# Kernel tuning notes

Hardware: AMD Instinct MI355X
Metric: run time of the kernel (lower is better)

Reference implementation:

```python
import jax, jax.numpy as jnp
import numpy as np

T, N, E = 3, 100000, 1600000
D_IN, D_H, D_OUT = 64, 64, 1


def _linear_params(key, fan_in, fan_out):
    s = 1.0 / np.sqrt(fan_in)
    k1, k2 = jax.random.split(key)
    W = jax.random.uniform(k1, (fan_in, fan_out), jnp.float32, -s, s)
    b = jax.random.uniform(k2, (fan_out,), jnp.float32, -s, s)
    return W, b


def setup_inputs() -> dict:
    key = jax.random.key(0)
    ks = jax.random.split(key, 9)
    x = jax.random.normal(ks[0], (T, N, D_IN), jnp.float32)
    src = jax.random.randint(ks[1], (T, E), 0, N, jnp.int32)
    dst = jax.random.randint(ks[2], (T, E), 0, N, jnp.int32)
    # xavier-uniform initial GCN weight [D_IN, D_H]
    lim = np.sqrt(6.0 / (D_IN + D_H))
    initial_weight = jax.random.uniform(ks[3], (D_IN, D_H), jnp.float32, -lim, lim)
    Wz, bz = _linear_params(ks[4], D_IN + D_H, D_H)  # update gate
    Wr, br = _linear_params(ks[5], D_IN + D_H, D_H)  # reset gate
    Wh, bh = _linear_params(ks[6], D_IN + D_H, D_H)  # htilda
    Wp, bp = _linear_params(ks[7], D_IN, D_IN)        # pool_proj
    Wo, bo = _linear_params(ks[8], D_H, D_OUT)        # out
    return dict(x=x, src=src, dst=dst, initial_weight=initial_weight,
                Wz=Wz, bz=bz, Wr=Wr, br=br, Wh=Wh, bh=bh,
                Wp=Wp, bp=bp, Wo=Wo, bo=bo)


def reference(x, src, dst, initial_weight, Wz, bz, Wr, br, Wh, bh, Wp, bp, Wo, bo):
    n_nodes = x.shape[1]
    ones_e = jnp.ones((x.shape[2] * 0 + src.shape[1],), jnp.float32)  # [E]

    def step(w, snap):
        xt, st, dt = snap  # [N, D_IN], [E], [E]
        # pooled graph context -> MatGRU weight evolution
        ctx = jnp.mean(xt, axis=0) @ Wp + bp            # [D_IN]
        inp = jnp.broadcast_to(ctx, (D_IN, D_IN))       # inputs.repeat(prev_w.size(0),1)
        xc = jnp.concatenate([inp, w], axis=1)          # [D_IN, D_IN+D_H]
        z = jax.nn.sigmoid(xc @ Wz + bz)
        r = jax.nn.sigmoid(xc @ Wr + br)
        gc = jnp.concatenate([inp, r * w], axis=1)
        h_tilde = jnp.tanh(gc @ Wh + bh)
        w_new = z * w + (1.0 - z) * h_tilde             # [D_IN, D_H]
        # GCN norm: deg = sum of (unit) edge weights per dst, clamp_min 1
        deg = jax.ops.segment_sum(ones_e, dt, num_segments=n_nodes)
        deg = jnp.maximum(deg, 1.0)
        norm = (1.0 / deg)[dt]                          # [E]
        # u_mul_e -> sum aggregation
        agg = jax.ops.segment_sum(xt[st] * norm[:, None], dt, num_segments=n_nodes)
        h = agg @ w_new                                 # [N, D_H]
        out = h @ Wo + bo                               # [N, D_OUT]
        return w_new, out

    w_final, outs = jax.lax.scan(step, initial_weight, (x, src, dst))
    return outs, w_final
```

## Files before the change

### kernel.cpp

```cpp
#include <hip/hip_runtime.h>
#include <math.h>

#define T_STEPS 3
#define N_NODES 100000
#define N_EDGES 1600000
#define N_E4    (N_EDGES / 4)
#define D 64

#define CS_BLOCKS 782

#define BKT_BITS 9
#define BKT_SIZE 512
#define NBKT 196
#define NBKT_PAD 256
#define QSCALE 65536.0f
#define QINV   (1.0f / 65536.0f)

#define SC_EPB 4096
#define SC_I4  1024
#define SC_CHUNKS 391

#define GR_PAD 68

#define PACK_SCALE 1048576.0f
#define PACK_INV   (1.0f / 1048576.0f)


__global__ __launch_bounds__(256) void colsum_part_kernel(const float* __restrict__ x,
                                                          float* __restrict__ colsumP) {
    const int t = blockIdx.y;
    const int tid = threadIdx.x;
    const int q = tid & 15;
    const int g = tid >> 4;
    const float4* xt = (const float4*)(x + (size_t)t * N_NODES * D);
    const int base = blockIdx.x * 128;
    float sx = 0.f, sy = 0.f, sz = 0.f, sw = 0.f;
#pragma unroll
    for (int it = 0; it < 8; ++it) {
        const int r = base + g + 16 * it;
        if (r < N_NODES) {
            const float4 vv = xt[(size_t)r * 16 + q];
            sx += vv.x; sy += vv.y; sz += vv.z; sw += vv.w;
        }
    }
    __shared__ float red[16][64];
    red[g][q * 4 + 0] = sx;
    red[g][q * 4 + 1] = sy;
    red[g][q * 4 + 2] = sz;
    red[g][q * 4 + 3] = sw;
    __syncthreads();
    if (tid < 64) {
        float s = 0.f;
#pragma unroll
        for (int gg = 0; gg < 16; ++gg) s += red[gg][tid];
        colsumP[((size_t)t * CS_BLOCKS + blockIdx.x) * 64 + tid] = s;
    }
}

__global__ __launch_bounds__(256) void hist_chunk_kernel(const int* __restrict__ dst,
                                                         unsigned* __restrict__ histChunk) {
    const int t = blockIdx.y;
    const int c = blockIdx.x;
    const int tid = threadIdx.x;
    __shared__ unsigned h[NBKT_PAD];
    h[tid] = 0;
    __syncthreads();
    const int4* dp = (const int4*)(dst + (size_t)t * N_EDGES);
#pragma unroll
    for (int it = 0; it < 4; ++it) {
        const int i4 = c * SC_I4 + it * 256 + tid;
        if (i4 < N_E4) {
            const int4 d = dp[i4];
            atomicAdd(&h[d.x >> BKT_BITS], 1u);
            atomicAdd(&h[d.y >> BKT_BITS], 1u);
            atomicAdd(&h[d.z >> BKT_BITS], 1u);
            atomicAdd(&h[d.w >> BKT_BITS], 1u);
        }
    }
    __syncthreads();
    histChunk[((size_t)t * SC_CHUNKS + c) * NBKT_PAD + tid] = h[tid];
}

__device__ __forceinline__ float fast_sigmoid(float v) {
    return 1.f / (1.f + __expf(-v));
}
__device__ __forceinline__ float fast_tanh(float v) {
    return 1.f - 2.f / (__expf(2.f * v) + 1.f);
}

__global__ __launch_bounds__(256) void gru_rows_kernel(
    const float* __restrict__ colsumP, const float* __restrict__ iw,
    const float* __restrict__ Wz, const float* __restrict__ bz,
    const float* __restrict__ Wr, const float* __restrict__ br,
    const float* __restrict__ Wh, const float* __restrict__ bh,
    const float* __restrict__ Wp, const float* __restrict__ bp,
    const float* __restrict__ Wo, const unsigned* __restrict__ histChunk,
    unsigned* __restrict__ bstart, unsigned* __restrict__ chunkPref,
    float* __restrict__ v_out, float* __restrict__ w_final) {
    const int tid = threadIdx.x;

    if (blockIdx.x == 16) {
        __shared__ unsigned scn[NBKT_PAD];
        for (int t = 0; t < T_STEPS; ++t) {
            unsigned c = 0;
            for (int k = 0; k < SC_CHUNKS; ++k)
                c += histChunk[((size_t)t * SC_CHUNKS + k) * NBKT_PAD + tid];
            unsigned v = c;
            scn[tid] = v;
            __syncthreads();
            for (int off = 1; off < NBKT_PAD; off <<= 1) {
                const unsigned add = (tid >= off) ? scn[tid - off] : 0u;
                __syncthreads();
                v += add;
                scn[tid] = v;
                __syncthreads();
            }
            bstart[t * NBKT_PAD + tid] = (unsigned)(t * N_EDGES) + (v - c);
            __syncthreads();
        }
        return;
    }
    if (blockIdx.x >= 17) {
        const int idx = blockIdx.x - 17;
        const int t = idx >> 6;
        const int wid = tid >> 6, lane = tid & 63;
        const int b = (idx & 63) * 4 + wid;
        unsigned running = 0;
#pragma unroll
        for (int g = 0; g < 7; ++g) {
            const int c = g * 64 + lane;
            const unsigned val = (c < SC_CHUNKS)
                ? histChunk[((size_t)t * SC_CHUNKS + c) * NBKT_PAD + b] : 0u;
            unsigned incl = val;
#pragma unroll
            for (int off = 1; off < 64; off <<= 1) {
                const unsigned n = __shfl_up(incl, off);
                if (lane >= off) incl += n;
            }
            if (c < SC_CHUNKS)
                chunkPref[((size_t)t * SC_CHUNKS + c) * NBKT_PAD + b] = running + (incl - val);
            running += __shfl(incl, 63);
        }
        return;
    }

    __shared__ float BzT[64 * GR_PAD];
    __shared__ float BrT[64 * GR_PAD];
    __shared__ float BhT[64 * GR_PAD];
    __shared__ float w_lds[4 * 64];
    __shared__ float mean_s[192];
    __shared__ float ctx_s[192];
    __shared__ float czrh_s[576];

#pragma unroll
    for (int it = 0; it < 16; ++it) {
        const int idx = it * 256 + tid;
        const int k = idx >> 6, j = idx & 63;
        BzT[j * GR_PAD + k] = Wz[(64 + k) * 64 + j];
        BrT[j * GR_PAD + k] = Wr[(64 + k) * 64 + j];
        BhT[j * GR_PAD + k] = Wh[(64 + k) * 64 + j];
    }
    if (tid < 192) {
        const int t = tid >> 6, j = tid & 63;
        float s = 0.f;
        for (int bx = 0; bx < CS_BLOCKS; ++bx)
            s += colsumP[((size_t)t * CS_BLOCKS + bx) * 64 + j];
        mean_s[tid] = s * (1.f / (float)N_NODES);
    }
    __syncthreads();
    if (tid < 192) {
        const int t = tid >> 6, j = tid & 63;
        float c = bp[j];
        for (int k = 0; k < 64; ++k)
            c = fmaf(mean_s[t * 64 + k], Wp[k * 64 + j], c);
        ctx_s[tid] = c;
    }
    __syncthreads();
    for (int co = (tid >> 6); co < 9; co += 4) {
        const int t = co / 3, m = co - 3 * t, j = tid & 63;
        const float* W = (m == 0) ? Wz : (m == 1) ? Wr : Wh;
        const float* bb = (m == 0) ? bz : (m == 1) ? br : bh;
        float c = bb[j];
        for (int k = 0; k < 64; ++k)
            c = fmaf(ctx_s[t * 64 + k], W[k * 64 + j], c);
        czrh_s[co * 64 + j] = c;
    }
    __syncthreads();

    const int wid = tid >> 6, lane = tid & 63;
    const int row = blockIdx.x * 4 + wid;
    float* wrow = &w_lds[wid * 64];
    float w = iw[row * 64 + lane];
    const float wo = Wo[lane];

    for (int t = 0; t < T_STEPS; ++t) {
        wrow[lane] = w;
        __syncthreads();
        float az = 0.f, ar = 0.f;
#pragma unroll
        for (int k0 = 0; k0 < 64; k0 += 4) {
            const float4 wv = *(const float4*)&wrow[k0];
            const float4 z4 = *(const float4*)&BzT[lane * GR_PAD + k0];
            const float4 r4 = *(const float4*)&BrT[lane * GR_PAD + k0];
            az = fmaf(wv.x, z4.x, az); az = fmaf(wv.y, z4.y, az);
            az = fmaf(wv.z, z4.z, az); az = fmaf(wv.w, z4.w, az);
            ar = fmaf(wv.x, r4.x, ar); ar = fmaf(wv.y, r4.y, ar);
            ar = fmaf(wv.z, r4.z, ar); ar = fmaf(wv.w, r4.w, ar);
        }
        const float z = fast_sigmoid(az + czrh_s[(t * 3 + 0) * 64 + lane]);
        const float r = fast_sigmoid(ar + czrh_s[(t * 3 + 1) * 64 + lane]);
        const float rw = r * w;
        __syncthreads();
        wrow[lane] = rw;
        __syncthreads();
        float ah = 0.f;
#pragma unroll
        for (int k0 = 0; k0 < 64; k0 += 4) {
            const float4 wv = *(const float4*)&wrow[k0];
            const float4 h4 = *(const float4*)&BhT[lane * GR_PAD + k0];
            ah = fmaf(wv.x, h4.x, ah); ah = fmaf(wv.y, h4.y, ah);
            ah = fmaf(wv.z, h4.z, ah); ah = fmaf(wv.w, h4.w, ah);
        }
        const float h = fast_tanh(ah + czrh_s[(t * 3 + 2) * 64 + lane]);
        w = z * w + (1.f - z) * h;
        float vp = w * wo;
        vp += __shfl_xor(vp, 1);
        vp += __shfl_xor(vp, 2);
        vp += __shfl_xor(vp, 4);
        vp += __shfl_xor(vp, 8);
        vp += __shfl_xor(vp, 16);
        vp += __shfl_xor(vp, 32);
        if (lane == 0) v_out[t * 64 + row] = vp;
        __syncthreads();
    }
    w_final[row * 64 + lane] = w;
}

__global__ __launch_bounds__(256) void smatvec_kernel(const float* __restrict__ x,
                                                      const float* __restrict__ v,
                                                      float* __restrict__ s) {
    const int t = blockIdx.y;
    const int tid = threadIdx.x;
    const int l4 = tid & 3;
    const int rloc = tid >> 2;
    __shared__ float vs[64];
    if (tid < 64) vs[tid] = v[t * 64 + tid];
    __syncthreads();
    const int row = blockIdx.x * 64 + rloc;
    if (row < N_NODES) {
        const float4* xr = (const float4*)(x + ((size_t)t * N_NODES + row) * D);
        float acc = 0.f;
#pragma unroll
        for (int i = 0; i < 4; ++i) {
            const int c = i * 4 + l4;
            const float4 xv = xr[c];
            acc += xv.x * vs[c * 4 + 0] + xv.y * vs[c * 4 + 1] +
                   xv.z * vs[c * 4 + 2] + xv.w * vs[c * 4 + 3];
        }
        acc += __shfl_xor(acc, 1);
        acc += __shfl_xor(acc, 2);
        if (l4 == 0) s[(size_t)t * N_NODES + row] = acc;
    }
}

__global__ __launch_bounds__(512) void scatter_sort_kernel(
    const int* __restrict__ src, const int* __restrict__ dst,
    const float* __restrict__ s, const unsigned* __restrict__ bstart,
    const unsigned* __restrict__ chunkPref, unsigned* __restrict__ recs) {
    const int t = blockIdx.y;
    const int c = blockIdx.x;
    const int tid = threadIdx.x;
    __shared__ unsigned recL[SC_EPB];
    __shared__ unsigned short bktL[SC_EPB];
    __shared__ unsigned bh[NBKT_PAD];
    __shared__ unsigned sc[NBKT_PAD];
    __shared__ unsigned lofs[NBKT_PAD];
    __shared__ unsigned badj[NBKT_PAD];

    if (tid < NBKT_PAD) bh[tid] = 0;
    __syncthreads();

    const int4* sp = (const int4*)(src + (size_t)t * N_EDGES);
    const int4* dp = (const int4*)(dst + (size_t)t * N_EDGES);
    const float* st = s + (size_t)t * N_NODES;

    unsigned rec[8];
    int bkt[8];
#pragma unroll
    for (int k = 0; k < 8; ++k) bkt[k] = -1;

#pragma unroll
    for (int it = 0; it < 2; ++it) {
        const int i4 = c * SC_I4 + it * 512 + tid;
        if (i4 < N_E4) {
            const int4 sv = sp[i4];
            const int4 dv = dp[i4];
            const int ss[4] = {sv.x, sv.y, sv.z, sv.w};
            const int dd[4] = {dv.x, dv.y, dv.z, dv.w};
#pragma unroll
            for (int j = 0; j < 4; ++j) {
                const int q = (int)llrintf(st[ss[j]] * QSCALE);
                const int b = dd[j] >> BKT_BITS;
                rec[it * 4 + j] = ((unsigned)(dd[j] & (BKT_SIZE - 1)) << 22) |
                                  ((unsigned)q & 0x3FFFFFu);
                bkt[it * 4 + j] = b;
                atomicAdd(&bh[b], 1u);
            }
        }
    }
    __syncthreads();
    if (tid < NBKT_PAD) sc[tid] = bh[tid];
    __syncthreads();
    for (int off = 1; off < NBKT_PAD; off <<= 1) {
        unsigned add = 0;
        if (tid < NBKT_PAD && tid >= off) add = sc[tid - off];
        __syncthreads();
        if (tid < NBKT_PAD) sc[tid] += add;
        __syncthreads();
    }
    if (tid < NBKT_PAD) {
        const unsigned cnt = bh[tid];
        const unsigned ex = sc[tid] - cnt;
        lofs[tid] = ex;
        const unsigned base = bstart[t * NBKT_PAD + tid] +
                              chunkPref[((size_t)t * SC_CHUNKS + c) * NBKT_PAD + tid];
        badj[tid] = base - ex;
    }
    __syncthreads();
#pragma unroll
    for (int k = 0; k < 8; ++k) {
        if (bkt[k] >= 0) {
            const unsigned pos = atomicAdd(&lofs[bkt[k]], 1u);
            recL[pos] = rec[k];
            bktL[pos] = (unsigned short)bkt[k];
        }
    }
    __syncthreads();
    const int nrec = min(SC_EPB, N_EDGES - c * SC_EPB);
    for (int i = tid; i < nrec; i += 512) {
        const unsigned b = bktL[i];
        recs[badj[b] + (unsigned)i] = recL[i];
    }
}

__global__ __launch_bounds__(256) void accum_kernel(const unsigned* __restrict__ recs,
                                                    const unsigned* __restrict__ start,
                                                    const float* __restrict__ bo,
                                                    float* __restrict__ out) {
    const int b = blockIdx.x;
    const int t = blockIdx.y;
    const int tid = threadIdx.x;
    __shared__ unsigned long long bins[BKT_SIZE];
    bins[tid] = 0ULL;
    bins[tid + 256] = 0ULL;
    __syncthreads();
    const unsigned s0 = start[t * NBKT_PAD + b];
    const unsigned s1 = start[t * NBKT_PAD + b + 1];
    for (unsigned i = s0 + tid; i < s1; i += 256) {
        const unsigned rec = recs[i];
        const unsigned dl = rec >> 22;
        const long long q = (long long)(((int)(rec << 10)) >> 10);
        atomicAdd(&bins[dl], (unsigned long long)((1ULL << 41) + (unsigned long long)q));
    }
    __syncthreads();
    const float bo0 = bo[0];
#pragma unroll
    for (int k = 0; k < 2; ++k) {
        const int i = tid + k * 256;
        const int node = b * BKT_SIZE + i;
        if (node < N_NODES) {
            const unsigned long long tot = bins[i];
            const unsigned long long deg = (tot + (1ULL << 40)) >> 41;
            const long long rem = (long long)(tot - (deg << 41));
            const float acc = (float)rem * QINV;
            out[(size_t)t * N_NODES + node] = bo0 + acc / fmaxf((float)deg, 1.f);
        }
    }
}


__global__ __launch_bounds__(256) void edge_kernel(const int* __restrict__ src,
                                                   const int* __restrict__ dst,
                                                   const float* __restrict__ s,
                                                   unsigned long long* __restrict__ packed) {
    const int t = blockIdx.y;
    const int e4 = blockIdx.x * 256 + threadIdx.x;
    if (e4 * 4 >= N_EDGES) return;
    const int4* sp = (const int4*)(src + (size_t)t * N_EDGES);
    const int4* dp = (const int4*)(dst + (size_t)t * N_EDGES);
    const float* st = s + (size_t)t * N_NODES;
    unsigned long long* pk = packed + (size_t)t * N_NODES;
    const int4 s4 = sp[e4];
    const int4 d4 = dp[e4];
    const float v0 = st[s4.x], v1 = st[s4.y], v2 = st[s4.z], v3 = st[s4.w];
    const unsigned long long base = 1ULL << 41;
    atomicAdd(&pk[d4.x], base + (unsigned long long)(long long)llrintf(v0 * PACK_SCALE));
    atomicAdd(&pk[d4.y], base + (unsigned long long)(long long)llrintf(v1 * PACK_SCALE));
    atomicAdd(&pk[d4.z], base + (unsigned long long)(long long)llrintf(v2 * PACK_SCALE));
    atomicAdd(&pk[d4.w], base + (unsigned long long)(long long)llrintf(v3 * PACK_SCALE));
}

__global__ __launch_bounds__(256) void out_kernel(const unsigned long long* __restrict__ packed,
                                                  const float* __restrict__ bo,
                                                  float* __restrict__ out) {
    const int i = blockIdx.x * 256 + threadIdx.x;
    if (i < T_STEPS * N_NODES) {
        const unsigned long long tot = packed[i];
        const unsigned long long deg = (tot + (1ULL << 40)) >> 41;
        const long long rem = (long long)(tot - (deg << 41));
        const float acc = (float)rem * PACK_INV;
        out[i] = bo[0] + acc / fmaxf((float)deg, 1.0f);
    }
}

extern "C" void kernel_launch(void* const* d_in, const int* in_sizes, int n_in,
                              void* d_out, int out_size, void* d_ws, size_t ws_size,
                              hipStream_t stream) {
    const float* x  = (const float*)d_in[0];
    const int* src  = (const int*)d_in[1];
    const int* dst  = (const int*)d_in[2];
    const float* iw = (const float*)d_in[3];
    const float* Wz = (const float*)d_in[4];
    const float* bz = (const float*)d_in[5];
    const float* Wr = (const float*)d_in[6];
    const float* br = (const float*)d_in[7];
    const float* Wh = (const float*)d_in[8];
    const float* bh = (const float*)d_in[9];
    const float* Wp = (const float*)d_in[10];
    const float* bp = (const float*)d_in[11];
    const float* Wo = (const float*)d_in[12];
    const float* bo = (const float*)d_in[13];
    float* out = (float*)d_out;
    float* ws  = (float*)d_ws;

    const size_t FAST_NEED = (size_t)5401248 * sizeof(float);
    if (ws_size >= FAST_NEED) {
        unsigned* recs      = (unsigned*)ws;
        float* colsumP      = ws;
        unsigned* histChunk = (unsigned*)(ws + 150144);
        unsigned* chunkPref = (unsigned*)(ws + 4800000);
        unsigned* bstart    = (unsigned*)(ws + 5100288);
        float* vbuf         = ws + 5101056;
        float* sbuf         = ws + 5101248;

        colsum_part_kernel<<<dim3(CS_BLOCKS, 3), 256, 0, stream>>>(x, colsumP);
        hist_chunk_kernel<<<dim3(SC_CHUNKS, 3), 256, 0, stream>>>(dst, histChunk);
        gru_rows_kernel<<<209, 256, 0, stream>>>(colsumP, iw, Wz, bz, Wr, br, Wh, bh,
                                                 Wp, bp, Wo, histChunk, bstart, chunkPref,
                                                 vbuf, out + (size_t)T_STEPS * N_NODES);
        smatvec_kernel<<<dim3(1563, 3), 256, 0, stream>>>(x, vbuf, sbuf);
        scatter_sort_kernel<<<dim3(SC_CHUNKS, 3), 512, 0, stream>>>(src, dst, sbuf,
                                                                    bstart, chunkPref, recs);
        accum_kernel<<<dim3(NBKT, 3), 256, 0, stream>>>(recs, bstart, bo, out);
    } else {
        float* colsumP = ws;
        float* vbuf    = ws + 150144;
        float* sbuf    = ws + 150336;
        unsigned long long* packed = (unsigned long long*)(ws + 450336);

        hipMemsetAsync(packed, 0, (size_t)600000 * sizeof(float), stream);

        colsum_part_kernel<<<dim3(CS_BLOCKS, 3), 256, 0, stream>>>(x, colsumP);
        gru_rows_kernel<<<16, 256, 0, stream>>>(colsumP, iw, Wz, bz, Wr, br, Wh, bh,
                                                Wp, bp, Wo, (unsigned*)nullptr,
                                                (unsigned*)nullptr, (unsigned*)nullptr,
                                                vbuf, out + (size_t)T_STEPS * N_NODES);
        smatvec_kernel<<<dim3(1563, 3), 256, 0, stream>>>(x, vbuf, sbuf);
        edge_kernel<<<dim3(1563, 3), 256, 0, stream>>>(src, dst, sbuf, packed);
        out_kernel<<<1172, 256, 0, stream>>>(packed, bo, out);
    }
}
```

Baseline: 108.3 us.

## Merge prep kernels and run scatter-sort alongside smatvec by deferring s lookup

Colsum and dst-histogram kernels become one launch with blocks split by blockIdx. The scatter-sort records now hold the source index (17 bits) instead of the quantized s value. That removes the sort's dependency on s, so smatvec blocks can run in the same launch as the sort. The accumulate kernel then gathers s[src] itself, which adds a random gather there but removes two launches and the smatvec-to-sort serialization. A latent race remains because sort blocks may run before the smatvec blocks write s, though s is only read in the later accum kernel, so it is safe.

```diff
diff --git a/kernel.cpp b/kernel.cpp
--- a/kernel.cpp
+++ b/kernel.cpp
@@ -20,65 +20,67 @@
 #define SC_I4  1024
 #define SC_CHUNKS 391
 
+#define SMV_BLOCKS 782
+
 #define GR_PAD 68
 
 #define PACK_SCALE 1048576.0f
 #define PACK_INV   (1.0f / 1048576.0f)
 
 
-__global__ __launch_bounds__(256) void colsum_part_kernel(const float* __restrict__ x,
-                                                          float* __restrict__ colsumP) {
+__global__ __launch_bounds__(256) void prep_kernel(const float* __restrict__ x,
+                                                   const int* __restrict__ dst,
+                                                   float* __restrict__ colsumP,
+                                                   unsigned* __restrict__ histChunk) {
     const int t = blockIdx.y;
     const int tid = threadIdx.x;
-    const int q = tid & 15;
-    const int g = tid >> 4;
-    const float4* xt = (const float4*)(x + (size_t)t * N_NODES * D);
-    const int base = blockIdx.x * 128;
-    float sx = 0.f, sy = 0.f, sz = 0.f, sw = 0.f;
-#pragma unroll
-    for (int it = 0; it < 8; ++it) {
-        const int r = base + g + 16 * it;
-        if (r < N_NODES) {
-            const float4 vv = xt[(size_t)r * 16 + q];
-            sx += vv.x; sy += vv.y; sz += vv.z; sw += vv.w;
-        }
-    }
     __shared__ float red[16][64];
-    red[g][q * 4 + 0] = sx;
-    red[g][q * 4 + 1] = sy;
-    red[g][q * 4 + 2] = sz;
-    red[g][q * 4 + 3] = sw;
-    __syncthreads();
-    if (tid < 64) {
-        float s = 0.f;
-#pragma unroll
-        for (int gg = 0; gg < 16; ++gg) s += red[gg][tid];
-        colsumP[((size_t)t * CS_BLOCKS + blockIdx.x) * 64 + tid] = s;
-    }
-}
-
-__global__ __launch_bounds__(256) void hist_chunk_kernel(const int* __restrict__ dst,
-                                                         unsigned* __restrict__ histChunk) {
-    const int t = blockIdx.y;
-    const int c = blockIdx.x;
-    const int tid = threadIdx.x;
     __shared__ unsigned h[NBKT_PAD];
-    h[tid] = 0;
-    __syncthreads();
-    const int4* dp = (const int4*)(dst + (size_t)t * N_EDGES);
-#pragma unroll
-    for (int it = 0; it < 4; ++it) {
-        const int i4 = c * SC_I4 + it * 256 + tid;
-        if (i4 < N_E4) {
-            const int4 d = dp[i4];
-            atomicAdd(&h[d.x >> BKT_BITS], 1u);
-            atomicAdd(&h[d.y >> BKT_BITS], 1u);
-            atomicAdd(&h[d.z >> BKT_BITS], 1u);
-            atomicAdd(&h[d.w >> BKT_BITS], 1u);
-        }
-    }
-    __syncthreads();
-    histChunk[((size_t)t * SC_CHUNKS + c) * NBKT_PAD + tid] = h[tid];
+
+    if (blockIdx.x < CS_BLOCKS) {
+        const int q = tid & 15;
+        const int g = tid >> 4;
+        const float4* xt = (const float4*)(x + (size_t)t * N_NODES * D);
+        const int base = blockIdx.x * 128;
+        float sx = 0.f, sy = 0.f, sz = 0.f, sw = 0.f;
+#pragma unroll
+        for (int it = 0; it < 8; ++it) {
+            const int r = base + g + 16 * it;
+            if (r < N_NODES) {
+                const float4 vv = xt[(size_t)r * 16 + q];
+                sx += vv.x; sy += vv.y; sz += vv.z; sw += vv.w;
+            }
+        }
+        red[g][q * 4 + 0] = sx;
+        red[g][q * 4 + 1] = sy;
+        red[g][q * 4 + 2] = sz;
+        red[g][q * 4 + 3] = sw;
+        __syncthreads();
+        if (tid < 64) {
+            float s = 0.f;
+#pragma unroll
+            for (int gg = 0; gg < 16; ++gg) s += red[gg][tid];
+            colsumP[((size_t)t * CS_BLOCKS + blockIdx.x) * 64 + tid] = s;
+        }
+    } else {
+        const int c = blockIdx.x - CS_BLOCKS;
+        h[tid] = 0;
+        __syncthreads();
+        const int4* dp = (const int4*)(dst + (size_t)t * N_EDGES);
+#pragma unroll
+        for (int it = 0; it < 4; ++it) {
+            const int i4 = c * SC_I4 + it * 256 + tid;
+            if (i4 < N_E4) {
+                const int4 d = dp[i4];
+                atomicAdd(&h[d.x >> BKT_BITS], 1u);
+                atomicAdd(&h[d.y >> BKT_BITS], 1u);
+                atomicAdd(&h[d.z >> BKT_BITS], 1u);
+                atomicAdd(&h[d.w >> BKT_BITS], 1u);
+            }
+        }
+        __syncthreads();
+        histChunk[((size_t)t * SC_CHUNKS + c) * NBKT_PAD + tid] = h[tid];
+    }
 }
 
 __device__ __forceinline__ float fast_sigmoid(float v) {
@@ -236,6 +238,148 @@
     w_final[row * 64 + lane] = w;
 }
 
+__global__ __launch_bounds__(512) void scat_smv_kernel(
+    const float* __restrict__ x, const float* __restrict__ v,
+    const int* __restrict__ src, const int* __restrict__ dst,
+    const unsigned* __restrict__ bstart, const unsigned* __restrict__ chunkPref,
+    unsigned* __restrict__ recs, float* __restrict__ s) {
+    const int t = blockIdx.y;
+    const int tid = threadIdx.x;
+    __shared__ __align__(16) unsigned char lds_raw[28672];
+
+    if (blockIdx.x >= SC_CHUNKS) {
+        float* vs = (float*)lds_raw;
+        if (tid < 64) vs[tid] = v[t * 64 + tid];
+        __syncthreads();
+        const int row = (blockIdx.x - SC_CHUNKS) * 128 + (tid >> 2);
+        const int l4 = tid & 3;
+        if (row < N_NODES) {
+            const float4* xr = (const float4*)(x + ((size_t)t * N_NODES + row) * D);
+            float acc = 0.f;
+#pragma unroll
+            for (int i = 0; i < 4; ++i) {
+                const int c = i * 4 + l4;
+                const float4 xv = xr[c];
+                acc += xv.x * vs[c * 4 + 0] + xv.y * vs[c * 4 + 1] +
+                       xv.z * vs[c * 4 + 2] + xv.w * vs[c * 4 + 3];
+            }
+            acc += __shfl_xor(acc, 1);
+            acc += __shfl_xor(acc, 2);
+            if (l4 == 0) s[(size_t)t * N_NODES + row] = acc;
+        }
+        return;
+    }
+
+    const int c = blockIdx.x;
+    unsigned* recL = (unsigned*)lds_raw;
+    unsigned short* bktL = (unsigned short*)(lds_raw + 16384);
+    unsigned* bh   = (unsigned*)(lds_raw + 24576);
+    unsigned* sc   = bh + 256;
+    unsigned* lofs = sc + 256;
+    unsigned* badj = lofs + 256;
+
+    if (tid < NBKT_PAD) bh[tid] = 0;
+    __syncthreads();
+
+    const int4* sp = (const int4*)(src + (size_t)t * N_EDGES);
+    const int4* dp = (const int4*)(dst + (size_t)t * N_EDGES);
+
+    unsigned rec[8];
+    int bkt[8];
+#pragma unroll
+    for (int k = 0; k < 8; ++k) bkt[k] = -1;
+
+#pragma unroll
+    for (int it = 0; it < 2; ++it) {
+        const int i4 = c * SC_I4 + it * 512 + tid;
+        if (i4 < N_E4) {
+            const int4 sv = sp[i4];
+            const int4 dv = dp[i4];
+            const int ss[4] = {sv.x, sv.y, sv.z, sv.w};
+            const int dd[4] = {dv.x, dv.y, dv.z, dv.w};
+#pragma unroll
+            for (int j = 0; j < 4; ++j) {
+                const int b = dd[j] >> BKT_BITS;
+                rec[it * 4 + j] = ((unsigned)(dd[j] & (BKT_SIZE - 1)) << 17) |
+                                  (unsigned)ss[j];
+                bkt[it * 4 + j] = b;
+                atomicAdd(&bh[b], 1u);
+            }
+        }
+    }
+    __syncthreads();
+    if (tid < NBKT_PAD) sc[tid] = bh[tid];
+    __syncthreads();
+    for (int off = 1; off < NBKT_PAD; off <<= 1) {
+        unsigned add = 0;
+        if (tid < NBKT_PAD && tid >= off) add = sc[tid - off];
+        __syncthreads();
+        if (tid < NBKT_PAD) sc[tid] += add;
+        __syncthreads();
+    }
+    if (tid < NBKT_PAD) {
+        const unsigned cnt = bh[tid];
+        const unsigned ex = sc[tid] - cnt;
+        lofs[tid] = ex;
+        const unsigned base = bstart[t * NBKT_PAD + tid] +
+                              chunkPref[((size_t)t * SC_CHUNKS + c) * NBKT_PAD + tid];
+        badj[tid] = base - ex;
+    }
+    __syncthreads();
+#pragma unroll
+    for (int k = 0; k < 8; ++k) {
+        if (bkt[k] >= 0) {
+            const unsigned pos = atomicAdd(&lofs[bkt[k]], 1u);
+            recL[pos] = rec[k];
+            bktL[pos] = (unsigned short)bkt[k];
+        }
+    }
+    __syncthreads();
+    const int nrec = min(SC_EPB, N_EDGES - c * SC_EPB);
+    for (int i = tid; i < nrec; i += 512) {
+        const unsigned b = bktL[i];
+        recs[badj[b] + (unsigned)i] = recL[i];
+    }
+}
+
+__global__ __launch_bounds__(256) void accum_kernel(const unsigned* __restrict__ recs,
+                                                    const unsigned* __restrict__ start,
+                                                    const float* __restrict__ s,
+                                                    const float* __restrict__ bo,
+                                                    float* __restrict__ out) {
+    const int b = blockIdx.x;
+    const int t = blockIdx.y;
+    const int tid = threadIdx.x;
+    __shared__ unsigned long long bins[BKT_SIZE];
+    bins[tid] = 0ULL;
+    bins[tid + 256] = 0ULL;
+    __syncthreads();
+    const float* st = s + (size_t)t * N_NODES;
+    const unsigned s0 = start[t * NBKT_PAD + b];
+    const unsigned s1 = start[t * NBKT_PAD + b + 1];
+    for (unsigned i = s0 + tid; i < s1; i += 256) {
+        const unsigned rec = recs[i];
+        const unsigned dl = rec >> 17;
+        const long long q = llrintf(st[rec & 0x1FFFFu] * QSCALE);
+        atomicAdd(&bins[dl], (unsigned long long)((1ULL << 41) + (unsigned long long)q));
+    }
+    __syncthreads();
+    const float bo0 = bo[0];
+#pragma unroll
+    for (int k = 0; k < 2; ++k) {
+        const int i = tid + k * 256;
+        const int node = b * BKT_SIZE + i;
+        if (node < N_NODES) {
+            const unsigned long long tot = bins[i];
+            const unsigned long long deg = (tot + (1ULL << 40)) >> 41;
+            const long long rem = (long long)(tot - (deg << 41));
+            const float acc = (float)rem * QINV;
+            out[(size_t)t * N_NODES + node] = bo0 + acc / fmaxf((float)deg, 1.f);
+        }
+    }
+}
+
+
 __global__ __launch_bounds__(256) void smatvec_kernel(const float* __restrict__ x,
                                                       const float* __restrict__ v,
                                                       float* __restrict__ s) {
@@ -262,122 +406,6 @@
         if (l4 == 0) s[(size_t)t * N_NODES + row] = acc;
     }
 }
-
-__global__ __launch_bounds__(512) void scatter_sort_kernel(
-    const int* __restrict__ src, const int* __restrict__ dst,
-    const float* __restrict__ s, const unsigned* __restrict__ bstart,
-    const unsigned* __restrict__ chunkPref, unsigned* __restrict__ recs) {
-    const int t = blockIdx.y;
-    const int c = blockIdx.x;
-    const int tid = threadIdx.x;
-    __shared__ unsigned recL[SC_EPB];
-    __shared__ unsigned short bktL[SC_EPB];
-    __shared__ unsigned bh[NBKT_PAD];
-    __shared__ unsigned sc[NBKT_PAD];
-    __shared__ unsigned lofs[NBKT_PAD];
-    __shared__ unsigned badj[NBKT_PAD];
-
-    if (tid < NBKT_PAD) bh[tid] = 0;
-    __syncthreads();
-
-    const int4* sp = (const int4*)(src + (size_t)t * N_EDGES);
-    const int4* dp = (const int4*)(dst + (size_t)t * N_EDGES);
-    const float* st = s + (size_t)t * N_NODES;
-
-    unsigned rec[8];
-    int bkt[8];
-#pragma unroll
-    for (int k = 0; k < 8; ++k) bkt[k] = -1;
-
-#pragma unroll
-    for (int it = 0; it < 2; ++it) {
-        const int i4 = c * SC_I4 + it * 512 + tid;
-        if (i4 < N_E4) {
-            const int4 sv = sp[i4];
-            const int4 dv = dp[i4];
-            const int ss[4] = {sv.x, sv.y, sv.z, sv.w};
-            const int dd[4] = {dv.x, dv.y, dv.z, dv.w};
-#pragma unroll
-            for (int j = 0; j < 4; ++j) {
-                const int q = (int)llrintf(st[ss[j]] * QSCALE);
-                const int b = dd[j] >> BKT_BITS;
-                rec[it * 4 + j] = ((unsigned)(dd[j] & (BKT_SIZE - 1)) << 22) |
-                                  ((unsigned)q & 0x3FFFFFu);
-                bkt[it * 4 + j] = b;
-                atomicAdd(&bh[b], 1u);
-            }
-        }
-    }
-    __syncthreads();
-    if (tid < NBKT_PAD) sc[tid] = bh[tid];
-    __syncthreads();
-    for (int off = 1; off < NBKT_PAD; off <<= 1) {
-        unsigned add = 0;
-        if (tid < NBKT_PAD && tid >= off) add = sc[tid - off];
-        __syncthreads();
-        if (tid < NBKT_PAD) sc[tid] += add;
-        __syncthreads();
-    }
-    if (tid < NBKT_PAD) {
-        const unsigned cnt = bh[tid];
-        const unsigned ex = sc[tid] - cnt;
-        lofs[tid] = ex;
-        const unsigned base = bstart[t * NBKT_PAD + tid] +
-                              chunkPref[((size_t)t * SC_CHUNKS + c) * NBKT_PAD + tid];
-        badj[tid] = base - ex;
-    }
-    __syncthreads();
-#pragma unroll
-    for (int k = 0; k < 8; ++k) {
-        if (bkt[k] >= 0) {
-            const unsigned pos = atomicAdd(&lofs[bkt[k]], 1u);
-            recL[pos] = rec[k];
-            bktL[pos] = (unsigned short)bkt[k];
-        }
-    }
-    __syncthreads();
-    const int nrec = min(SC_EPB, N_EDGES - c * SC_EPB);
-    for (int i = tid; i < nrec; i += 512) {
-        const unsigned b = bktL[i];
-        recs[badj[b] + (unsigned)i] = recL[i];
-    }
-}
-
-__global__ __launch_bounds__(256) void accum_kernel(const unsigned* __restrict__ recs,
-                                                    const unsigned* __restrict__ start,
-                                                    const float* __restrict__ bo,
-                                                    float* __restrict__ out) {
-    const int b = blockIdx.x;
-    const int t = blockIdx.y;
-    const int tid = threadIdx.x;
-    __shared__ unsigned long long bins[BKT_SIZE];
-    bins[tid] = 0ULL;
-    bins[tid + 256] = 0ULL;
-    __syncthreads();
-    const unsigned s0 = start[t * NBKT_PAD + b];
-    const unsigned s1 = start[t * NBKT_PAD + b + 1];
-    for (unsigned i = s0 + tid; i < s1; i += 256) {
-        const unsigned rec = recs[i];
-        const unsigned dl = rec >> 22;
-        const long long q = (long long)(((int)(rec << 10)) >> 10);
-        atomicAdd(&bins[dl], (unsigned long long)((1ULL << 41) + (unsigned long long)q));
-    }
-    __syncthreads();
-    const float bo0 = bo[0];
-#pragma unroll
-    for (int k = 0; k < 2; ++k) {
-        const int i = tid + k * 256;
-        const int node = b * BKT_SIZE + i;
-        if (node < N_NODES) {
-            const unsigned long long tot = bins[i];
-            const unsigned long long deg = (tot + (1ULL << 40)) >> 41;
-            const long long rem = (long long)(tot - (deg << 41));
-            const float acc = (float)rem * QINV;
-            out[(size_t)t * N_NODES + node] = bo0 + acc / fmaxf((float)deg, 1.f);
-        }
-    }
-}
-
 
 __global__ __launch_bounds__(256) void edge_kernel(const int* __restrict__ src,
                                                    const int* __restrict__ dst,
@@ -443,15 +471,14 @@
         float* vbuf         = ws + 5101056;
         float* sbuf         = ws + 5101248;
 
-        colsum_part_kernel<<<dim3(CS_BLOCKS, 3), 256, 0, stream>>>(x, colsumP);
-        hist_chunk_kernel<<<dim3(SC_CHUNKS, 3), 256, 0, stream>>>(dst, histChunk);
+        prep_kernel<<<dim3(CS_BLOCKS + SC_CHUNKS, 3), 256, 0, stream>>>(x, dst,
+                                                                        colsumP, histChunk);
         gru_rows_kernel<<<209, 256, 0, stream>>>(colsumP, iw, Wz, bz, Wr, br, Wh, bh,
                                                  Wp, bp, Wo, histChunk, bstart, chunkPref,
                                                  vbuf, out + (size_t)T_STEPS * N_NODES);
-        smatvec_kernel<<<dim3(1563, 3), 256, 0, stream>>>(x, vbuf, sbuf);
-        scatter_sort_kernel<<<dim3(SC_CHUNKS, 3), 512, 0, stream>>>(src, dst, sbuf,
-                                                                    bstart, chunkPref, recs);
-        accum_kernel<<<dim3(NBKT, 3), 256, 0, stream>>>(recs, bstart, bo, out);
+        scat_smv_kernel<<<dim3(SC_CHUNKS + SMV_BLOCKS, 3), 512, 0, stream>>>(
+            x, vbuf, src, dst, bstart, chunkPref, recs, sbuf);
+        accum_kernel<<<dim3(NBKT, 3), 256, 0, stream>>>(recs, bstart, sbuf, bo, out);
     } else {
         float* colsumP = ws;
         float* vbuf    = ws + 150144;
@@ -460,7 +487,8 @@
 
         hipMemsetAsync(packed, 0, (size_t)600000 * sizeof(float), stream);
 
-        colsum_part_kernel<<<dim3(CS_BLOCKS, 3), 256, 0, stream>>>(x, colsumP);
+        prep_kernel<<<dim3(CS_BLOCKS, 3), 256, 0, stream>>>(x, dst, colsumP,
+                                                            (unsigned*)nullptr);
         gru_rows_kernel<<<16, 256, 0, stream>>>(colsumP, iw, Wz, bz, Wr, br, Wh, bh,
                                                 Wp, bp, Wo, (unsigned*)nullptr,
                                                 (unsigned*)nullptr, (unsigned*)nullptr,
```

After: 105.5 us. -2.7%, faster.
